# Kernel tuning notes

Hardware: AMD Instinct MI355X
Metric: run time of the kernel (lower is better)

Reference implementation:

```python
import jax, jax.numpy as jnp
import numpy as np

WIN, DIL, PAD, H = 5, 1, 2, 8  # window, dilation, unfold padding, num_heads
C = 256
EPS = 1e-5

def _ln(z, g, b):
    m = jnp.mean(z, axis=-1, keepdims=True)
    v = jnp.mean((z - m) ** 2, axis=-1, keepdims=True)
    return (z - m) * jax.lax.rsqrt(v + EPS) * g + b

def setup_inputs() -> dict:
    key = jax.random.key(0)
    ks = jax.random.split(key, 16)
    s = 0.02
    d = {
        'x': jax.random.normal(ks[0], (32, C, 64, 25), jnp.float32),
        'ln1_g': jnp.ones((C,), jnp.float32), 'ln1_b': jnp.zeros((C,), jnp.float32),
        'q_w': jax.random.normal(ks[1], (C, C)) * s, 'q_b': jnp.zeros((C,)),
        'qa_w': jax.random.normal(ks[2], (C, H)) * s, 'qa_b': jnp.zeros((H,)),
        'k_w': jax.random.normal(ks[3], (C, C)) * s, 'k_b': jnp.zeros((C,)),
        'ka_w': jax.random.normal(ks[4], (C, H)) * s, 'ka_b': jnp.zeros((H,)),
        'v_w': jax.random.normal(ks[5], (C, C)) * s, 'v_b': jnp.zeros((C,)),
        't_w': jax.random.normal(ks[6], (C, C)) * s, 't_b': jnp.zeros((C,)),
        'p_w': jax.random.normal(ks[7], (C, C)) * s, 'p_b': jnp.zeros((C,)),
        'ffn_g': jnp.ones((C,)), 'ffn_b': jnp.zeros((C,)),
        'w1': jax.random.normal(ks[8], (C, C)) * s, 'b1': jnp.zeros((C,)),
        'w2': jax.random.normal(ks[9], (C, C)) * s, 'b2': jnp.zeros((C,)),
    }
    return d

def reference(x, ln1_g, ln1_b, q_w, q_b, qa_w, qa_b, k_w, k_b, ka_w, ka_b,
              v_w, v_b, t_w, t_b, p_w, p_b, ffn_g, ffn_b, w1, b1, w2, b2):
    N, Cc, T, V = x.shape
    hc = Cc // H
    scale = 1.0 / np.sqrt(hc)
    B, L = N * T, WIN * V
    xp = jnp.pad(x, ((0, 0), (0, 0), (PAD, PAD), (0, 0)))
    win = jnp.stack([xp[:, :, k * DIL:k * DIL + T, :] for k in range(WIN)], axis=2)  # (N,C,W,T,V)
    wx = win.transpose(0, 3, 2, 4, 1).reshape(B, L, Cc)
    nx = _ln(wx, ln1_g, ln1_b)
    # attention: softmax-pooled query
    q = nx @ q_w + q_b                                      # (B,L,C)
    qw = jax.nn.softmax(((q @ qa_w + qa_b) * scale).transpose(0, 2, 1), axis=-1)  # (B,H,L)
    qh = q.reshape(B, L, H, hc).transpose(0, 2, 1, 3)       # (B,H,L,hc)
    pq = jnp.einsum('bhl,bhld->bhd', qw, qh)                # (B,H,hc)
    k_ = nx @ k_w + k_b
    kq = k_ * pq.reshape(B, 1, Cc)
    kw = jax.nn.softmax(((kq @ ka_w + ka_b) * scale).transpose(0, 2, 1), axis=-1)
    kh = k_.reshape(B, L, H, hc).transpose(0, 2, 1, 3)
    pk = jnp.einsum('bhl,bhld->bhd', kw, kh)                # (B,H,hc)
    v_ = nx @ v_w + v_b
    vh = v_.reshape(B, L, H, hc).transpose(0, 2, 1, 3)
    kv = (vh * pk[:, :, None, :]).transpose(0, 2, 1, 3).reshape(B, L, Cc)
    kvh = (kv @ t_w + t_b).reshape(B, L, H, hc).transpose(0, 2, 1, 3)
    att = ((kvh + qh).transpose(0, 2, 1, 3).reshape(B, L, Cc)) @ p_w + p_b
    # average over window, residual with flattened x
    att = att.reshape(B, WIN, V, Cc).mean(axis=1)           # (B,V,C)
    att = att + x.transpose(0, 2, 3, 1).reshape(B, V, Cc)
    # FFN residual block
    f = _ln(att, ffn_g, ffn_b)
    f = jax.nn.gelu(f @ w1 + b1, approximate=False) @ w2 + b2
    y = f + att
    return y.reshape(N, T, V, Cc).transpose(0, 3, 1, 2)     # (N,C,T,V)
```

## Files before the change

### kernel.cpp

```cpp
#include <hip/hip_runtime.h>
#include <hip/hip_bf16.h>

typedef unsigned short u16b;
typedef __attribute__((ext_vector_type(8))) short short8;
typedef __attribute__((ext_vector_type(4))) float floatx4;

#define DEV static __device__ __forceinline__

DEV float sh2f(unsigned short s) { union { unsigned u; float f; } c; c.u = ((unsigned)s) << 16; return c.f; }
DEV unsigned short f2b(float f) {
    unsigned u = __float_as_uint(f);
    u += 0x7FFF + ((u >> 16) & 1);
    return (unsigned short)(u >> 16);
}

DEV void gload_lds16(const u16b* g, u16b* l) {
    __builtin_amdgcn_global_load_lds((const __attribute__((address_space(1))) void*)g,
                                     (__attribute__((address_space(3))) void*)l, 16, 0, 0);
}

constexpr int O_LN1G = 0, O_LN1B = 256, O_QB = 512, O_KB = 768, O_VB = 1024,
              O_TB = 1280, O_PB = 1536, O_FFNG = 1792, O_FFNB = 2048,
              O_B1 = 2304, O_B2 = 2560, O_QAB = 2816, O_KAB = 2824,
              O_QAW = 2832, O_KAW = 4880, O_CV = 6928;
constexpr int VALIDC = 51200;

__global__ void detect_k(const unsigned* __restrict__ xw, int* __restrict__ flag) {
    __shared__ int cnt;
    if (threadIdx.x == 0) cnt = 0;
    __syncthreads();
    int my = 0;
    for (int i = threadIdx.x; i < 4096; i += 256) {
        unsigned w = xw[i];
        unsigned e0 = (w >> 7) & 0xFFu;
        if (e0 >= 0xC0u) my++;
    }
    atomicAdd(&cnt, my);
    __syncthreads();
    if (threadIdx.x == 0) flag[0] = (cnt > 64) ? 1 : 0;
}

DEV unsigned short load_cvt(const void* src, size_t idx, int fp32) {
    return fp32 ? f2b(((const float*)src)[idx]) : ((const u16b*)src)[idx];
}

struct VecTab { const void* p[15]; int off[15]; int n[15]; };

__global__ __launch_bounds__(256)
void convert_vecs_k(VecTab tab, const int* __restrict__ flag, u16b* __restrict__ sv) {
    int e = blockIdx.x, fp32 = flag[0];
    const void* s = tab.p[e];
    int n = tab.n[e], off = tab.off[e];
    for (int i = threadIdx.x; i < n; i += 256)
        sv[off + i] = load_cvt(s, i, fp32);
}

struct W8 { const void* p[8]; unsigned dstoff[8]; unsigned rstride[8]; };

__global__ void wtrans_k(W8 tab, u16b* __restrict__ base, const int* __restrict__ flag) {
    __shared__ u16b tile[32][33];
    int fp32 = flag[0];
    const void* src = tab.p[blockIdx.z];
    u16b* dst = base + tab.dstoff[blockIdx.z];
    unsigned rs = tab.rstride[blockIdx.z];
    int c0 = blockIdx.x * 32, r0 = blockIdx.y * 32;
    int tx = threadIdx.x, ty = threadIdx.y;
#pragma unroll
    for (int i = 0; i < 32; i += 8)
        tile[ty + i][tx] = load_cvt(src, (size_t)(r0 + ty + i) * 256 + c0 + tx, fp32);
    __syncthreads();
#pragma unroll
    for (int i = 0; i < 32; i += 8)
        dst[(size_t)(c0 + ty + i) * rs + r0 + tx] = tile[tx][ty + i];
}

__global__ __launch_bounds__(256)
void transpose_in_k(const void* __restrict__ src, u16b* __restrict__ dst,
                    int rows, int cols, const int* __restrict__ flag) {
    __shared__ u16b tile[32][36];
    int fp32 = flag[0];
    int c0 = blockIdx.x * 32, r0 = blockIdx.y * 32;
    size_t zb = (size_t)blockIdx.z * rows * cols;
    int tid = threadIdx.x;
    int r = tid >> 3, c4 = (tid & 7) * 4;
    size_t sidx = zb + (size_t)(r0 + r) * cols + c0 + c4;
    if (fp32) {
        const float4 f4 = *(const float4*)((const float*)src + sidx);
        tile[r][c4]     = f2b(f4.x);
        tile[r][c4 + 1] = f2b(f4.y);
        tile[r][c4 + 2] = f2b(f4.z);
        tile[r][c4 + 3] = f2b(f4.w);
    } else {
        *(ushort4*)&tile[r][c4] = *(const ushort4*)((const u16b*)src + sidx);
    }
    __syncthreads();
    int c = tid >> 3, r4 = (tid & 7) * 4;
    ushort4 o;
    o.x = tile[r4][c]; o.y = tile[r4 + 1][c]; o.z = tile[r4 + 2][c]; o.w = tile[r4 + 3][c];
    *(ushort4*)&dst[zb + (size_t)(c0 + c) * rows + r0 + r4] = o;
}

__global__ __launch_bounds__(256)
void cvec_k(const u16b* __restrict__ pT, u16b* __restrict__ sv) {
    int j = threadIdx.x;
    float acc = sh2f(sv[O_PB + j]);
    const u16b* row = pT + (size_t)j * 256;
    for (int i = 0; i < 256; i += 8) {
        short8 t8 = *(const short8*)&sv[O_TB + i];
        short8 p8 = *(const short8*)&row[i];
#pragma unroll
        for (int u = 0; u < 8; ++u)
            acc += sh2f((unsigned short)t8[u]) * sh2f((unsigned short)p8[u]);
    }
    sv[O_CV + j] = f2b(acc);
}

template <int EPI, int LNA, int XY = 0, int STATS = 0>
__global__ __launch_bounds__(256, 4)
void gemm256(const u16b* __restrict__ A, int aStride, int K,
             const u16b* __restrict__ Wt,
             const u16b* __restrict__ bias, const u16b* __restrict__ addm,
             u16b* __restrict__ out, size_t osParam,
             const float2* __restrict__ stats, const float2* __restrict__ stats2,
             const u16b* __restrict__ gvec, const u16b* __restrict__ bvec,
             float2* __restrict__ statOut, const int* __restrict__ flag) {
    constexpr bool ALDS = (LNA == 0);
    __shared__ u16b As[64 * 72];
    __shared__ u16b Bs[8448];
    __shared__ float sg[256], sb[256];
    const int tid = threadIdx.x;
    const int m0 = (XY ? blockIdx.y : blockIdx.x) * 64;
    const int n0 = (XY ? blockIdx.x : blockIdx.y) * 128;
    const int wv = tid >> 6, lane = tid & 63;
    const int wrow = (wv >> 1) * 32, wcol = (wv & 1) * 64;
    const int fr = lane & 15;
    const int fq = lane >> 4;
    floatx4 acc[2][4];
    const floatx4 zero = {0.f, 0.f, 0.f, 0.f};
#pragma unroll
    for (int i = 0; i < 2; ++i)
#pragma unroll
        for (int j = 0; j < 4; ++j) acc[i][j] = zero;

    float2 strow[2];
    if (LNA) {
        sg[tid] = sh2f(gvec[tid]);
        sb[tid] = sh2f(bvec[tid]);
        if (LNA == 1) {
#pragma unroll
            for (int kk = 0; kk < 2; ++kk) {
                int chunk = tid + kk * 256;
                int row = chunk >> 3, col = (chunk & 7) * 8;
                float s1 = 0.f, s2 = 0.f;
#pragma unroll
                for (int kt2 = 0; kt2 < 256; kt2 += 64) {
                    union { uint4 u; unsigned short h[8]; } rw;
                    rw.u = *(const uint4*)&A[(size_t)(m0 + row) * aStride + kt2 + col];
#pragma unroll
                    for (int j = 0; j < 8; ++j) {
                        float f = sh2f(rw.h[j]);
                        s1 += f; s2 += f * f;
                    }
                }
#pragma unroll
                for (int mm = 1; mm < 8; mm <<= 1) {
                    s1 += __shfl_xor(s1, mm);
                    s2 += __shfl_xor(s2, mm);
                }
                float mean = s1 * (1.f / 256.f);
                float var  = s2 * (1.f / 256.f) - mean * mean;
                strow[kk] = (m0 + row < VALIDC) ? make_float2(mean, rsqrtf(var + 1e-5f))
                                                : make_float2(0.f, 0.f);
            }
        } else {
#pragma unroll
            for (int kk = 0; kk < 2; ++kk) {
                int r = m0 + (tid >> 3) + kk * 32;
                float2 a = stats[r], b = stats2[r];
                float mean = (a.x + b.x) * (1.f / 256.f);
                float var  = (a.y + b.y) * (1.f / 256.f) - mean * mean;
                strow[kk] = make_float2(mean, rsqrtf(var + 1e-5f));
            }
        }
        __syncthreads();
    }

    for (int kt = 0; kt < K; kt += 64) {
        if (ALDS) {
#pragma unroll
            for (int kk = 0; kk < 2; ++kk) {
                int chunk = tid + kk * 256;
                int row = chunk >> 3, col = (chunk & 7) * 8;
                int scol = col ^ ((row & 7) << 3);
                gload_lds16(&A[(size_t)(m0 + row) * aStride + kt + scol], &As[chunk * 8]);
            }
        } else {
#pragma unroll
            for (int kk = 0; kk < 2; ++kk) {
                int chunk = tid + kk * 256;
                int row = chunk >> 3, col = (chunk & 7) * 8;
                union { uint4 u; unsigned short h[8]; } rw;
                rw.u = *(const uint4*)&A[(size_t)(m0 + row) * aStride + kt + col];
#pragma unroll
                for (int j = 0; j < 8; ++j) {
                    float f = sh2f(rw.h[j]);
                    f = (f - strow[kk].x) * strow[kk].y * sg[kt + col + j] + sb[kt + col + j];
                    rw.h[j] = f2b(f);
                }
                *(uint4*)&As[row * 72 + col] = rw.u;
            }
        }
#pragma unroll
        for (int kk = 0; kk < 4; ++kk) {
            int chunk = tid + kk * 256;
            int row = chunk >> 3, col = (chunk & 7) * 8;
            int scol = col ^ ((row & 7) << 3);
            gload_lds16(&Wt[(size_t)(n0 + row) * K + kt + scol], &Bs[chunk * 8]);
        }
        __syncthreads();
#pragma unroll
        for (int s = 0; s < 2; ++s) {
            short8 af[2], bfr[4];
#pragma unroll
            for (int i = 0; i < 2; ++i) {
                int ar = wrow + i * 16 + fr;
                if (ALDS)
                    af[i] = *(const short8*)((const char*)As +
                              ((ar * 128 + s * 64 + fq * 16) ^ ((ar & 7) << 4)));
                else
                    af[i] = *(short8*)&As[ar * 72 + s * 32 + fq * 8];
            }
#pragma unroll
            for (int j = 0; j < 4; ++j) {
                int br = wcol + j * 16 + fr;
                bfr[j] = *(const short8*)((const char*)Bs +
                          ((br * 128 + s * 64 + fq * 16) ^ ((br & 7) << 4)));
            }
#pragma unroll
            for (int i = 0; i < 2; ++i)
#pragma unroll
                for (int j = 0; j < 4; ++j)
                    acc[i][j] = __builtin_amdgcn_mfma_f32_16x16x32_bf16(af[i], bfr[j], acc[i][j], 0, 0, 0);
        }
        __syncthreads();
    }
    float bv[4];
#pragma unroll
    for (int j = 0; j < 4; ++j) bv[j] = bias ? sh2f(bias[n0 + wcol + j * 16 + fr]) : 0.f;

    if (EPI == 5) {
        u16b* CT = Bs;
#pragma unroll
        for (int kk = 0; kk < 4; ++kk) {
            int chunk = tid + kk * 256;
            int row = chunk >> 4, c8 = (chunk & 15) * 8;
            *(uint4*)&CT[row * 132 + c8] = *(const uint4*)&addm[(size_t)(m0 + row) * 256 + n0 + c8];
        }
        __syncthreads();
        int fp32o = flag[0];
#pragma unroll
        for (int i = 0; i < 2; ++i) {
            int lr0 = wrow + i * 16 + fq * 4;
            int row0 = m0 + lr0;
            int n = row0 / 1600;
            int tv = row0 - n * 1600;
#pragma unroll
            for (int j = 0; j < 4; ++j) {
                int lc = wcol + j * 16 + fr;
                int col = n0 + lc;
                float v4[4];
#pragma unroll
                for (int r = 0; r < 4; ++r)
                    v4[r] = acc[i][j][r] + bv[j] + sh2f(CT[(lr0 + r) * 132 + lc]);
                size_t oidx = ((size_t)n * 256 + col) * 1600 + tv;
                if (fp32o) {
                    float4 o = {v4[0], v4[1], v4[2], v4[3]};
                    *(float4*)((float*)out + oidx) = o;
                } else {
                    ushort4 o;
                    o.x = f2b(v4[0]); o.y = f2b(v4[1]); o.z = f2b(v4[2]); o.w = f2b(v4[3]);
                    *(ushort4*)&out[oidx] = o;
                }
            }
        }
    } else if (EPI == 2) {
        float* CTf = (float*)Bs;
#pragma unroll
        for (int half = 0; half < 2; ++half) {
            if ((wrow >> 5) == half) {
#pragma unroll
                for (int i = 0; i < 2; ++i)
#pragma unroll
                    for (int r = 0; r < 4; ++r) {
                        int lrow = i * 16 + fq * 4 + r;
#pragma unroll
                        for (int j = 0; j < 4; ++j)
                            CTf[lrow * 132 + wcol + j * 16 + fr] = acc[i][j][r] + bv[j];
                    }
            }
            __syncthreads();
#pragma unroll
            for (int kk = 0; kk < 2; ++kk) {
                int chunk = tid + kk * 256;
                int row = chunk >> 4, c8 = (chunk & 15) * 8;
                int grow = m0 + half * 32 + row, gcol = n0 + c8;
                union { uint4 u; unsigned short h[8]; } am, ow;
                am.u = *(const uint4*)&addm[(size_t)grow * 256 + gcol];
                float s1 = 0.f, s2 = 0.f;
#pragma unroll
                for (int u8 = 0; u8 < 8; ++u8) {
                    float v = CTf[row * 132 + c8 + u8] + sh2f(am.h[u8]);
                    s1 += v; s2 += v * v;
                    ow.h[u8] = f2b(v);
                }
                if (STATS) {
#pragma unroll
                    for (int mm = 1; mm < 16; mm <<= 1) {
                        s1 += __shfl_xor(s1, mm);
                        s2 += __shfl_xor(s2, mm);
                    }
                    if ((tid & 15) == 0)
                        statOut[(size_t)(n0 >> 7) * 51200 + grow] = make_float2(s1, s2);
                }
                *(uint4*)&out[(size_t)grow * 256 + gcol] = ow.u;
            }
            __syncthreads();
        }
    } else {
        u16b* CT = Bs;
#pragma unroll
        for (int i = 0; i < 2; ++i)
#pragma unroll
            for (int r = 0; r < 4; ++r) {
                int lrow = wrow + i * 16 + fq * 4 + r;
#pragma unroll
                for (int j = 0; j < 4; ++j) {
                    float val = acc[i][j][r] + bv[j];
                    if (EPI == 3) val = 0.5f * val * (1.0f + erff(val * 0.70710678118654752f));
                    CT[lrow * 132 + wcol + j * 16 + fr] = f2b(val);
                }
            }
        __syncthreads();
#pragma unroll
        for (int kk = 0; kk < 4; ++kk) {
            int chunk = tid + kk * 256;
            int row = chunk >> 4, c8 = (chunk & 15) * 8;
            int grow = m0 + row, gcol = n0 + c8;
            uint4 cw = *(const uint4*)&CT[row * 132 + c8];
            if (EPI == 4)      *(uint4*)&out[(size_t)(gcol >> 8) * osParam + (size_t)grow * 256 + (gcol & 255)] = cw;
            else               *(uint4*)&out[(size_t)grow * osParam + gcol] = cw;
        }
    }
}


DEV void logits_union(const u16b* __restrict__ S, const u16b* su, const int* srow,
                      float* slog, const u16b* __restrict__ sv, int aboff, int tid) {
    int wv = tid >> 6, lane = tid & 63;
    int fr = lane & 15, fq = lane >> 4;
    float abv = sh2f(sv[aboff + (fr & 7)]);
    for (int f = wv; f < 10; f += 8) {
        floatx4 acc = {0.f, 0.f, 0.f, 0.f};
        const u16b* Ar = S + (size_t)srow[f * 16 + fr] * 256;
#pragma unroll
        for (int s = 0; s < 8; ++s) {
            short8 a  = *(const short8*)&Ar[s * 32 + fq * 8];
            short8 bb = *(const short8*)&su[fr * 260 + s * 32 + fq * 8];
            acc = __builtin_amdgcn_mfma_f32_16x16x32_bf16(a, bb, acc, 0, 0, 0);
        }
#pragma unroll
        for (int r = 0; r < 4; ++r)
            slog[(f * 16 + fq * 4 + r) * 19 + fr] = (acc[r] + abv) * 0.17677669529663687f;
    }
}

template <int KC>
DEV void softmax16(const float* slog, float* wqA, float* wqB, int tid) {
    int wv = tid >> 6, lane = tid & 63;
#pragma unroll
    for (int c = 0; c < 2; ++c) {
        int combo = wv + c * 8;
        int dt = combo >> 3, h = combo & 7;
        int col = KC ? combo : h;
        const float* src = slog + (size_t)(dt * 25) * 19 + col;
        float v0 = (lane < 125) ? src[lane * 19] : -1e30f;
        float v1 = (lane + 64 < 125) ? src[(lane + 64) * 19] : -1e30f;
        float mx = fmaxf(v0, v1);
#pragma unroll
        for (int o = 32; o; o >>= 1) mx = fmaxf(mx, __shfl_xor(mx, o));
        float e0 = (lane < 125) ? __expf(v0 - mx) : 0.f;
        float e1 = (lane + 64 < 125) ? __expf(v1 - mx) : 0.f;
        float s = e0 + e1;
#pragma unroll
        for (int o = 32; o; o >>= 1) s += __shfl_xor(s, o);
        float inv = 1.f / s;
        float* dst = dt ? wqB : wqA;
        int off = dt ? 25 : 0;
        if (lane < 125) dst[(lane + off) * 9 + h] = e0 * inv;
        if (lane + 64 < 125) dst[(lane + 64 + off) * 9 + h] = e1 * inv;
    }
}

DEV void pool_sweep2(const u16b* __restrict__ S, const int* srow,
                     const float* wqA, const float* wqB,
                     float* scrA, float* scrB, int tid) {
    int c8 = (tid & 31) * 8, h = c8 >> 5, ls = tid >> 5;
    float a0[8] = {0.f,0.f,0.f,0.f,0.f,0.f,0.f,0.f};
    float a1[8] = {0.f,0.f,0.f,0.f,0.f,0.f,0.f,0.f};
    for (int u = ls; u < 150; u += 16) {
        float w0 = wqA[u * 9 + h];
        float w1 = wqB[u * 9 + h];
        short8 d8 = *(const short8*)&S[(size_t)srow[u] * 256 + c8];
#pragma unroll
        for (int j = 0; j < 8; ++j) {
            float f = sh2f((unsigned short)d8[j]);
            a0[j] += w0 * f;
            a1[j] += w1 * f;
        }
    }
#pragma unroll
    for (int j = 0; j < 8; ++j) {
        a0[j] += __shfl_xor(a0[j], 32);
        a1[j] += __shfl_xor(a1[j], 32);
    }
    int wv = tid >> 6, lane = tid & 63;
    if (lane < 32) {
        float4 lo0 = {a0[0], a0[1], a0[2], a0[3]}, hi0 = {a0[4], a0[5], a0[6], a0[7]};
        *(float4*)&scrA[wv * 264 + c8]     = lo0;
        *(float4*)&scrA[wv * 264 + c8 + 4] = hi0;
        float4 lo1 = {a1[0], a1[1], a1[2], a1[3]}, hi1 = {a1[4], a1[5], a1[6], a1[7]};
        *(float4*)&scrB[wv * 260 + c8]     = lo1;
        *(float4*)&scrB[wv * 260 + c8 + 4] = hi1;
    }
}

DEV void pool_reduce2(const float* scrA, const float* scrB,
                      float* out0, float* out1, int tid) {
    if (tid < 256) {
        float s = 0.f;
#pragma unroll
        for (int q = 0; q < 8; ++q) s += scrA[q * 264 + tid];
        out0[tid] = s;
    } else {
        int t2 = tid - 256;
        float s = 0.f;
#pragma unroll
        for (int q = 0; q < 8; ++q) s += scrB[q * 260 + t2];
        out1[t2] = s;
    }
}

DEV void wmean2(const u16b* __restrict__ S, const int* srow,
                const float* scale0, const float* scale1,
                u16b* __restrict__ CB, int base, int nb, int tid) {
    for (int i = tid; i < 800; i += 512) {
        int v = i >> 5, c8 = (i & 31) * 8;
        float s0[8] = {0.f,0.f,0.f,0.f,0.f,0.f,0.f,0.f};
        float s1[8] = {0.f,0.f,0.f,0.f,0.f,0.f,0.f,0.f};
#pragma unroll
        for (int w = 0; w < 6; ++w) {
            short8 d8 = *(const short8*)&S[(size_t)srow[w * 25 + v] * 256 + c8];
#pragma unroll
            for (int j = 0; j < 8; ++j) {
                float f = sh2f((unsigned short)d8[j]);
                if (w < 5)  s0[j] += f;
                if (w >= 1) s1[j] += f;
            }
        }
        unsigned short o0[8], o1[8];
#pragma unroll
        for (int j = 0; j < 8; ++j) {
            float m0 = s0[j] * 0.2f, m1 = s1[j] * 0.2f;
            if (scale0) { m0 *= scale0[c8 + j]; m1 *= scale1[c8 + j]; }
            o0[j] = f2b(m0); o1[j] = f2b(m1);
        }
        *(uint4*)&CB[((size_t)nb * 25 + v) * 512 + base + c8]       = *(uint4*)o0;
        *(uint4*)&CB[((size_t)(nb + 1) * 25 + v) * 512 + base + c8] = *(uint4*)o1;
    }
}

__global__ __launch_bounds__(512)
void pool_fused2(const u16b* __restrict__ qf, const u16b* __restrict__ kf,
                 const u16b* __restrict__ vf, const u16b* __restrict__ sv,
                 u16b* __restrict__ CB) {
    __shared__ int srow[160];
    __shared__ alignas(16) u16b su[16 * 260];
    __shared__ float slog[160 * 19];
    __shared__ float wqA[160 * 9], wqB[160 * 9];
    __shared__ float spq[2][256], spk[2][256];
    int bid = blockIdx.x;
    int b2 = ((bid & 7) << 7) | (bid >> 3);
    int n = b2 >> 5, t0 = (b2 & 31) * 2;
    int nb = n * 64 + t0;
    int tid = threadIdx.x;
    if (tid < 160) {
        int u = tid < 150 ? tid : 149;
        int tl = u / 25, v = u - tl * 25, tt = t0 + tl - 2;
        srow[tid] = ((unsigned)tt < 64u) ? (n * 64 + tt) * 25 + v : 51200;
    }
    for (int i = tid; i < 2048; i += 512) {
        int c = i >> 3, h = i & 7;
        su[h * 260 + c] = sv[O_QAW + i];
    }
    for (int i = tid; i < 1440; i += 512) { wqA[i] = 0.f; wqB[i] = 0.f; }
    __syncthreads();

    logits_union(qf, su, srow, slog, sv, O_QAB, tid);
    __syncthreads();
    softmax16<0>(slog, wqA, wqB, tid);
    __syncthreads();

    pool_sweep2(qf, srow, wqA, wqB, slog, (float*)su, tid);
    wmean2(qf, srow, nullptr, nullptr, CB, 256, nb, tid);
    __syncthreads();
    pool_reduce2(slog, (float*)su, spq[0], spq[1], tid);
    __syncthreads();

    for (int i = tid; i < 4096; i += 512) {
        int c = i >> 4, h16 = i & 15;
        float w = sh2f(sv[O_KAW + c * 8 + (h16 & 7)]) * spq[h16 >> 3][c];
        su[h16 * 260 + c] = f2b(w);
    }
    __syncthreads();

    logits_union(kf, su, srow, slog, sv, O_KAB, tid);
    __syncthreads();
    softmax16<1>(slog, wqA, wqB, tid);
    __syncthreads();

    pool_sweep2(kf, srow, wqA, wqB, slog, (float*)su, tid);
    __syncthreads();
    pool_reduce2(slog, (float*)su, spk[0], spk[1], tid);
    __syncthreads();

    wmean2(vf, srow, spk[0], spk[1], CB, 0, nb, tid);
}

extern "C" void kernel_launch(void* const* d_in, const int* in_sizes, int n_in,
                              void* d_out, int out_size, void* d_ws, size_t ws_size,
                              hipStream_t stream) {
    (void)in_sizes; (void)n_in; (void)out_size; (void)ws_size;
    const void* x    = d_in[0];
    const void* ln1g = d_in[1];  const void* ln1b = d_in[2];
    const void* q_w  = d_in[3];  const void* q_b  = d_in[4];
    const void* qa_w = d_in[5];  const void* qa_b = d_in[6];
    const void* k_w  = d_in[7];  const void* k_b  = d_in[8];
    const void* ka_w = d_in[9];  const void* ka_b = d_in[10];
    const void* v_w  = d_in[11]; const void* v_b  = d_in[12];
    const void* t_w  = d_in[13]; const void* t_b  = d_in[14];
    const void* p_w  = d_in[15]; const void* p_b  = d_in[16];
    const void* ffng = d_in[17]; const void* ffnb = d_in[18];
    const void* w1   = d_in[19]; const void* b1   = d_in[20];
    const void* w2   = d_in[21]; const void* b2   = d_in[22];

    char* ws = (char*)d_ws;
    size_t off = 0;
    auto alloc = [&](size_t bytes) { void* p = ws + off; off += (bytes + 255) & ~(size_t)255; return p; };
    const size_t RPAD = 51328;
    int*    flag = (int*)alloc(256);
    u16b*   sv   = (u16b*)alloc(8192 * 2);
    u16b*   wT   = (u16b*)alloc((size_t)7 * 65536 * 2);
    u16b*   cW   = (u16b*)alloc((size_t)256 * 512 * 2);
    u16b*   xT   = (u16b*)alloc(RPAD * 256 * 2);
    u16b*   Bq   = (u16b*)alloc(RPAD * 256 * 2);
    u16b*   Bk   = (u16b*)alloc(RPAD * 256 * 2);
    u16b*   Bv   = (u16b*)alloc(RPAD * 256 * 2);
    u16b*   CB   = (u16b*)alloc((size_t)51200 * 512 * 2);
    u16b*   att  = (u16b*)alloc((size_t)51200 * 256 * 2);
    float2* st2p = (float2*)alloc((size_t)2 * 51200 * 8);

    u16b* pT  = wT + 3 * 65536;
    u16b* tT  = wT + 4 * 65536;
    u16b* w1T = wT + 5 * 65536;
    u16b* w2T = wT + 6 * 65536;

    detect_k<<<1, 256, 0, stream>>>((const unsigned*)x, flag);
    VecTab tab;
    const void* vp[15] = {ln1g, ln1b, q_b, k_b, v_b, t_b, p_b, ffng, ffnb, b1, b2, qa_b, ka_b, qa_w, ka_w};
    const int vo[15] = {O_LN1G, O_LN1B, O_QB, O_KB, O_VB, O_TB, O_PB, O_FFNG, O_FFNB, O_B1, O_B2, O_QAB, O_KAB, O_QAW, O_KAW};
    const int vn[15] = {256, 256, 256, 256, 256, 256, 256, 256, 256, 256, 256, 8, 8, 2048, 2048};
    for (int i = 0; i < 15; ++i) { tab.p[i] = vp[i]; tab.off[i] = vo[i]; tab.n[i] = vn[i]; }
    convert_vecs_k<<<15, 256, 0, stream>>>(tab, flag, sv);

    dim3 tb(32, 8);
    W8 wt;
    const void* wsrc[8] = {q_w, k_w, v_w, p_w, t_w, w1, w2, p_w};
    for (int i = 0; i < 8; ++i) {
        wt.p[i] = wsrc[i];
        wt.dstoff[i] = (i < 7) ? (unsigned)(i * 65536) : (unsigned)((cW + 256) - wT);
        wt.rstride[i] = (i < 7) ? 256u : 512u;
    }
    wtrans_k<<<dim3(8, 8, 8), tb, 0, stream>>>(wt, wT, flag);
    cvec_k<<<1, 256, 0, stream>>>(pT, sv);
    gemm256<0, 0><<<dim3(4, 2), 256, 0, stream>>>(pT, 256, 256, tT, nullptr, nullptr,
                                                  cW, 512, nullptr, nullptr, nullptr, nullptr,
                                                  nullptr, nullptr);
    transpose_in_k<<<dim3(50, 8, 32), 256, 0, stream>>>(x, xT, 256, 1600, flag);
    gemm256<4, 1, 1><<<dim3(6, 802), 256, 0, stream>>>(xT, 256, 256, wT, sv + O_QB, nullptr,
                                                       Bq, RPAD * 256, nullptr, nullptr,
                                                       sv + O_LN1G, sv + O_LN1B, nullptr, nullptr);
    pool_fused2<<<1024, 512, 0, stream>>>(Bq, Bk, Bv, sv, CB);
    gemm256<2, 0, 1, 1><<<dim3(2, 800), 256, 0, stream>>>(CB, 512, 512, cW, sv + O_CV, xT,
                                                          att, 256, nullptr, nullptr,
                                                          nullptr, nullptr, st2p, nullptr);
    gemm256<3, 2, 1><<<dim3(2, 800), 256, 0, stream>>>(att, 256, 256, w1T, sv + O_B1, nullptr,
                                                       Bq, 256, st2p, st2p + 51200,
                                                       sv + O_FFNG, sv + O_FFNB, nullptr, nullptr);
    gemm256<5, 0, 1><<<dim3(2, 800), 256, 0, stream>>>(Bq, 256, 256, w2T, sv + O_B2, att,
                                                       (u16b*)d_out, 0, nullptr, nullptr,
                                                       nullptr, nullptr, nullptr, flag);
}
```

Measured before the change: 370.8 us.

## Fuse FFN LayerNorm, both GEMMs, GELU and residual into one kernel

Replaces the two separate FFN GEMM launches (LN+W1+GELU, then W2+residual+transposed output) with a single kernel that keeps a 64x256 row tile in LDS. It normalizes att, computes the hidden activations, applies GELU back into LDS, then runs the second GEMM and writes the output. This avoids the round trip of the hidden tensor through global memory and one kernel launch. In exchange each block handles the full 256 output columns, so the grid has fewer, larger blocks with more LDS and registers, which lowers occupancy and re-streams both weight matrices per block.

```diff
diff --git a/kernel.cpp b/kernel.cpp
--- a/kernel.cpp
+++ b/kernel.cpp
@@ -121,9 +121,8 @@
              const u16b* __restrict__ Wt,
              const u16b* __restrict__ bias, const u16b* __restrict__ addm,
              u16b* __restrict__ out, size_t osParam,
-             const float2* __restrict__ stats, const float2* __restrict__ stats2,
              const u16b* __restrict__ gvec, const u16b* __restrict__ bvec,
-             float2* __restrict__ statOut, const int* __restrict__ flag) {
+             float2* __restrict__ statOut) {
     constexpr bool ALDS = (LNA == 0);
     __shared__ u16b As[64 * 72];
     __shared__ u16b Bs[8448];
@@ -146,41 +145,30 @@
     if (LNA) {
         sg[tid] = sh2f(gvec[tid]);
         sb[tid] = sh2f(bvec[tid]);
-        if (LNA == 1) {
-#pragma unroll
-            for (int kk = 0; kk < 2; ++kk) {
-                int chunk = tid + kk * 256;
-                int row = chunk >> 3, col = (chunk & 7) * 8;
-                float s1 = 0.f, s2 = 0.f;
-#pragma unroll
-                for (int kt2 = 0; kt2 < 256; kt2 += 64) {
-                    union { uint4 u; unsigned short h[8]; } rw;
-                    rw.u = *(const uint4*)&A[(size_t)(m0 + row) * aStride + kt2 + col];
-#pragma unroll
-                    for (int j = 0; j < 8; ++j) {
-                        float f = sh2f(rw.h[j]);
-                        s1 += f; s2 += f * f;
-                    }
+#pragma unroll
+        for (int kk = 0; kk < 2; ++kk) {
+            int chunk = tid + kk * 256;
+            int row = chunk >> 3, col = (chunk & 7) * 8;
+            float s1 = 0.f, s2 = 0.f;
+#pragma unroll
+            for (int kt2 = 0; kt2 < 256; kt2 += 64) {
+                union { uint4 u; unsigned short h[8]; } rw;
+                rw.u = *(const uint4*)&A[(size_t)(m0 + row) * aStride + kt2 + col];
+#pragma unroll
+                for (int j = 0; j < 8; ++j) {
+                    float f = sh2f(rw.h[j]);
+                    s1 += f; s2 += f * f;
                 }
-#pragma unroll
-                for (int mm = 1; mm < 8; mm <<= 1) {
-                    s1 += __shfl_xor(s1, mm);
-                    s2 += __shfl_xor(s2, mm);
-                }
-                float mean = s1 * (1.f / 256.f);
-                float var  = s2 * (1.f / 256.f) - mean * mean;
-                strow[kk] = (m0 + row < VALIDC) ? make_float2(mean, rsqrtf(var + 1e-5f))
-                                                : make_float2(0.f, 0.f);
-            }
-        } else {
-#pragma unroll
-            for (int kk = 0; kk < 2; ++kk) {
-                int r = m0 + (tid >> 3) + kk * 32;
-                float2 a = stats[r], b = stats2[r];
-                float mean = (a.x + b.x) * (1.f / 256.f);
-                float var  = (a.y + b.y) * (1.f / 256.f) - mean * mean;
-                strow[kk] = make_float2(mean, rsqrtf(var + 1e-5f));
-            }
+            }
+#pragma unroll
+            for (int mm = 1; mm < 8; mm <<= 1) {
+                s1 += __shfl_xor(s1, mm);
+                s2 += __shfl_xor(s2, mm);
+            }
+            float mean = s1 * (1.f / 256.f);
+            float var  = s2 * (1.f / 256.f) - mean * mean;
+            strow[kk] = (m0 + row < VALIDC) ? make_float2(mean, rsqrtf(var + 1e-5f))
+                                            : make_float2(0.f, 0.f);
         }
         __syncthreads();
     }
@@ -248,16 +236,225 @@
 #pragma unroll
     for (int j = 0; j < 4; ++j) bv[j] = bias ? sh2f(bias[n0 + wcol + j * 16 + fr]) : 0.f;
 
-    if (EPI == 5) {
+    if (EPI == 2) {
+        float* CTf = (float*)Bs;
+#pragma unroll
+        for (int half = 0; half < 2; ++half) {
+            if ((wrow >> 5) == half) {
+#pragma unroll
+                for (int i = 0; i < 2; ++i)
+#pragma unroll
+                    for (int r = 0; r < 4; ++r) {
+                        int lrow = i * 16 + fq * 4 + r;
+#pragma unroll
+                        for (int j = 0; j < 4; ++j)
+                            CTf[lrow * 132 + wcol + j * 16 + fr] = acc[i][j][r] + bv[j];
+                    }
+            }
+            __syncthreads();
+#pragma unroll
+            for (int kk = 0; kk < 2; ++kk) {
+                int chunk = tid + kk * 256;
+                int row = chunk >> 4, c8 = (chunk & 15) * 8;
+                int grow = m0 + half * 32 + row, gcol = n0 + c8;
+                union { uint4 u; unsigned short h[8]; } am, ow;
+                am.u = *(const uint4*)&addm[(size_t)grow * 256 + gcol];
+                float s1 = 0.f, s2 = 0.f;
+#pragma unroll
+                for (int u8 = 0; u8 < 8; ++u8) {
+                    float v = CTf[row * 132 + c8 + u8] + sh2f(am.h[u8]);
+                    s1 += v; s2 += v * v;
+                    ow.h[u8] = f2b(v);
+                }
+                if (STATS) {
+#pragma unroll
+                    for (int mm = 1; mm < 16; mm <<= 1) {
+                        s1 += __shfl_xor(s1, mm);
+                        s2 += __shfl_xor(s2, mm);
+                    }
+                    if ((tid & 15) == 0)
+                        statOut[(size_t)(n0 >> 7) * 51200 + grow] = make_float2(s1, s2);
+                }
+                *(uint4*)&out[(size_t)grow * 256 + gcol] = ow.u;
+            }
+            __syncthreads();
+        }
+    } else {
         u16b* CT = Bs;
+#pragma unroll
+        for (int i = 0; i < 2; ++i)
+#pragma unroll
+            for (int r = 0; r < 4; ++r) {
+                int lrow = wrow + i * 16 + fq * 4 + r;
+#pragma unroll
+                for (int j = 0; j < 4; ++j)
+                    CT[lrow * 132 + wcol + j * 16 + fr] = f2b(acc[i][j][r] + bv[j]);
+            }
+        __syncthreads();
 #pragma unroll
         for (int kk = 0; kk < 4; ++kk) {
             int chunk = tid + kk * 256;
             int row = chunk >> 4, c8 = (chunk & 15) * 8;
-            *(uint4*)&CT[row * 132 + c8] = *(const uint4*)&addm[(size_t)(m0 + row) * 256 + n0 + c8];
-        }
-        __syncthreads();
-        int fp32o = flag[0];
+            int grow = m0 + row, gcol = n0 + c8;
+            uint4 cw = *(const uint4*)&CT[row * 132 + c8];
+            if (EPI == 4)      *(uint4*)&out[(size_t)(gcol >> 8) * osParam + (size_t)grow * 256 + (gcol & 255)] = cw;
+            else               *(uint4*)&out[(size_t)grow * osParam + gcol] = cw;
+        }
+    }
+}
+
+__global__ __launch_bounds__(256, 3)
+void ffn_fused(const u16b* __restrict__ att, const u16b* __restrict__ w1t,
+               const u16b* __restrict__ w2t, const u16b* __restrict__ sv,
+               const float2* __restrict__ stats, const float2* __restrict__ stats2,
+               u16b* __restrict__ out, const int* __restrict__ flag) {
+    __shared__ u16b AT[64 * 264];
+    __shared__ u16b Bs[8448];
+    __shared__ float sg[256], sb[256];
+    const int tid = threadIdx.x;
+    const int m0 = blockIdx.x * 64;
+    const int wv = tid >> 6, lane = tid & 63;
+    const int wrow = (wv >> 1) * 32, wcol = (wv & 1) * 64;
+    const int fr = lane & 15, fq = lane >> 4;
+    const floatx4 zero = {0.f, 0.f, 0.f, 0.f};
+
+    sg[tid] = sh2f(sv[O_FFNG + tid]);
+    sb[tid] = sh2f(sv[O_FFNB + tid]);
+    __syncthreads();
+
+#pragma unroll
+    for (int kk = 0; kk < 8; ++kk) {
+        int chunk = tid + kk * 256;
+        int row = chunk >> 5, col = (chunk & 31) * 8;
+        float2 a = stats[m0 + row], b = stats2[m0 + row];
+        float mean = (a.x + b.x) * (1.f / 256.f);
+        float var  = (a.y + b.y) * (1.f / 256.f) - mean * mean;
+        float rstd = rsqrtf(var + 1e-5f);
+        union { uint4 u; unsigned short h[8]; } rw;
+        rw.u = *(const uint4*)&att[(size_t)(m0 + row) * 256 + col];
+#pragma unroll
+        for (int j = 0; j < 8; ++j) {
+            float f = sh2f(rw.h[j]);
+            f = (f - mean) * rstd * sg[col + j] + sb[col + j];
+            rw.h[j] = f2b(f);
+        }
+        *(uint4*)&AT[row * 264 + col] = rw.u;
+    }
+    __syncthreads();
+
+    floatx4 acc[2][2][4];
+#pragma unroll
+    for (int H = 0; H < 2; ++H)
+#pragma unroll
+        for (int i = 0; i < 2; ++i)
+#pragma unroll
+            for (int j = 0; j < 4; ++j) acc[H][i][j] = zero;
+
+#pragma unroll
+    for (int H = 0; H < 2; ++H) {
+        for (int kt = 0; kt < 256; kt += 64) {
+#pragma unroll
+            for (int kk = 0; kk < 4; ++kk) {
+                int chunk = tid + kk * 256;
+                int row = chunk >> 3, col = (chunk & 7) * 8;
+                int scol = col ^ ((row & 7) << 3);
+                gload_lds16(&w1t[(size_t)(H * 128 + row) * 256 + kt + scol], &Bs[chunk * 8]);
+            }
+            __syncthreads();
+#pragma unroll
+            for (int s = 0; s < 2; ++s) {
+                short8 af[2], bfr[4];
+#pragma unroll
+                for (int i = 0; i < 2; ++i)
+                    af[i] = *(short8*)&AT[(wrow + i * 16 + fr) * 264 + kt + s * 32 + fq * 8];
+#pragma unroll
+                for (int j = 0; j < 4; ++j) {
+                    int br = wcol + j * 16 + fr;
+                    bfr[j] = *(const short8*)((const char*)Bs +
+                              ((br * 128 + s * 64 + fq * 16) ^ ((br & 7) << 4)));
+                }
+#pragma unroll
+                for (int i = 0; i < 2; ++i)
+#pragma unroll
+                    for (int j = 0; j < 4; ++j)
+                        acc[H][i][j] = __builtin_amdgcn_mfma_f32_16x16x32_bf16(af[i], bfr[j], acc[H][i][j], 0, 0, 0);
+            }
+            __syncthreads();
+        }
+    }
+#pragma unroll
+    for (int H = 0; H < 2; ++H) {
+        float bv1[4];
+#pragma unroll
+        for (int j = 0; j < 4; ++j) bv1[j] = sh2f(sv[O_B1 + H * 128 + wcol + j * 16 + fr]);
+#pragma unroll
+        for (int i = 0; i < 2; ++i)
+#pragma unroll
+            for (int r = 0; r < 4; ++r) {
+                int lrow = wrow + i * 16 + fq * 4 + r;
+#pragma unroll
+                for (int j = 0; j < 4; ++j) {
+                    float val = acc[H][i][j][r] + bv1[j];
+                    val = 0.5f * val * (1.0f + erff(val * 0.70710678118654752f));
+                    AT[lrow * 264 + H * 128 + wcol + j * 16 + fr] = f2b(val);
+                }
+            }
+    }
+    __syncthreads();
+
+    floatx4 acc2[2][2][4];
+#pragma unroll
+    for (int H = 0; H < 2; ++H)
+#pragma unroll
+        for (int i = 0; i < 2; ++i)
+#pragma unroll
+            for (int j = 0; j < 4; ++j) acc2[H][i][j] = zero;
+
+#pragma unroll
+    for (int H = 0; H < 2; ++H) {
+        for (int kt = 0; kt < 256; kt += 64) {
+#pragma unroll
+            for (int kk = 0; kk < 4; ++kk) {
+                int chunk = tid + kk * 256;
+                int row = chunk >> 3, col = (chunk & 7) * 8;
+                int scol = col ^ ((row & 7) << 3);
+                gload_lds16(&w2t[(size_t)(H * 128 + row) * 256 + kt + scol], &Bs[chunk * 8]);
+            }
+            __syncthreads();
+#pragma unroll
+            for (int s = 0; s < 2; ++s) {
+                short8 af[2], bfr[4];
+#pragma unroll
+                for (int i = 0; i < 2; ++i)
+                    af[i] = *(short8*)&AT[(wrow + i * 16 + fr) * 264 + kt + s * 32 + fq * 8];
+#pragma unroll
+                for (int j = 0; j < 4; ++j) {
+                    int br = wcol + j * 16 + fr;
+                    bfr[j] = *(const short8*)((const char*)Bs +
+                              ((br * 128 + s * 64 + fq * 16) ^ ((br & 7) << 4)));
+                }
+#pragma unroll
+                for (int i = 0; i < 2; ++i)
+#pragma unroll
+                    for (int j = 0; j < 4; ++j)
+                        acc2[H][i][j] = __builtin_amdgcn_mfma_f32_16x16x32_bf16(af[i], bfr[j], acc2[H][i][j], 0, 0, 0);
+            }
+            __syncthreads();
+        }
+    }
+#pragma unroll
+    for (int kk = 0; kk < 8; ++kk) {
+        int chunk = tid + kk * 256;
+        int row = chunk >> 5, c8 = (chunk & 31) * 8;
+        *(uint4*)&AT[row * 264 + c8] = *(const uint4*)&att[(size_t)(m0 + row) * 256 + c8];
+    }
+    __syncthreads();
+    int fp32o = flag[0];
+#pragma unroll
+    for (int H = 0; H < 2; ++H) {
+        float bv2[4];
+#pragma unroll
+        for (int j = 0; j < 4; ++j) bv2[j] = sh2f(sv[O_B2 + H * 128 + wcol + j * 16 + fr]);
 #pragma unroll
         for (int i = 0; i < 2; ++i) {
             int lr0 = wrow + i * 16 + fq * 4;
@@ -266,13 +463,12 @@
             int tv = row0 - n * 1600;
 #pragma unroll
             for (int j = 0; j < 4; ++j) {
-                int lc = wcol + j * 16 + fr;
-                int col = n0 + lc;
+                int lc = H * 128 + wcol + j * 16 + fr;
                 float v4[4];
 #pragma unroll
                 for (int r = 0; r < 4; ++r)
-                    v4[r] = acc[i][j][r] + bv[j] + sh2f(CT[(lr0 + r) * 132 + lc]);
-                size_t oidx = ((size_t)n * 256 + col) * 1600 + tv;
+                    v4[r] = acc2[H][i][j][r] + bv2[j] + sh2f(AT[(lr0 + r) * 264 + lc]);
+                size_t oidx = ((size_t)n * 256 + lc) * 1600 + tv;
                 if (fp32o) {
                     float4 o = {v4[0], v4[1], v4[2], v4[3]};
                     *(float4*)((float*)out + oidx) = o;
@@ -282,73 +478,6 @@
                     *(ushort4*)&out[oidx] = o;
                 }
             }
-        }
-    } else if (EPI == 2) {
-        float* CTf = (float*)Bs;
-#pragma unroll
-        for (int half = 0; half < 2; ++half) {
-            if ((wrow >> 5) == half) {
-#pragma unroll
-                for (int i = 0; i < 2; ++i)
-#pragma unroll
-                    for (int r = 0; r < 4; ++r) {
-                        int lrow = i * 16 + fq * 4 + r;
-#pragma unroll
-                        for (int j = 0; j < 4; ++j)
-                            CTf[lrow * 132 + wcol + j * 16 + fr] = acc[i][j][r] + bv[j];
-                    }
-            }
-            __syncthreads();
-#pragma unroll
-            for (int kk = 0; kk < 2; ++kk) {
-                int chunk = tid + kk * 256;
-                int row = chunk >> 4, c8 = (chunk & 15) * 8;
-                int grow = m0 + half * 32 + row, gcol = n0 + c8;
-                union { uint4 u; unsigned short h[8]; } am, ow;
-                am.u = *(const uint4*)&addm[(size_t)grow * 256 + gcol];
-                float s1 = 0.f, s2 = 0.f;
-#pragma unroll
-                for (int u8 = 0; u8 < 8; ++u8) {
-                    float v = CTf[row * 132 + c8 + u8] + sh2f(am.h[u8]);
-                    s1 += v; s2 += v * v;
-                    ow.h[u8] = f2b(v);
-                }
-                if (STATS) {
-#pragma unroll
-                    for (int mm = 1; mm < 16; mm <<= 1) {
-                        s1 += __shfl_xor(s1, mm);
-                        s2 += __shfl_xor(s2, mm);
-                    }
-                    if ((tid & 15) == 0)
-                        statOut[(size_t)(n0 >> 7) * 51200 + grow] = make_float2(s1, s2);
-                }
-                *(uint4*)&out[(size_t)grow * 256 + gcol] = ow.u;
-            }
-            __syncthreads();
-        }
-    } else {
-        u16b* CT = Bs;
-#pragma unroll
-        for (int i = 0; i < 2; ++i)
-#pragma unroll
-            for (int r = 0; r < 4; ++r) {
-                int lrow = wrow + i * 16 + fq * 4 + r;
-#pragma unroll
-                for (int j = 0; j < 4; ++j) {
-                    float val = acc[i][j][r] + bv[j];
-                    if (EPI == 3) val = 0.5f * val * (1.0f + erff(val * 0.70710678118654752f));
-                    CT[lrow * 132 + wcol + j * 16 + fr] = f2b(val);
-                }
-            }
-        __syncthreads();
-#pragma unroll
-        for (int kk = 0; kk < 4; ++kk) {
-            int chunk = tid + kk * 256;
-            int row = chunk >> 4, c8 = (chunk & 15) * 8;
-            int grow = m0 + row, gcol = n0 + c8;
-            uint4 cw = *(const uint4*)&CT[row * 132 + c8];
-            if (EPI == 4)      *(uint4*)&out[(size_t)(gcol >> 8) * osParam + (size_t)grow * 256 + (gcol & 255)] = cw;
-            else               *(uint4*)&out[(size_t)grow * osParam + gcol] = cw;
         }
     }
 }
@@ -593,20 +722,14 @@
     wtrans_k<<<dim3(8, 8, 8), tb, 0, stream>>>(wt, wT, flag);
     cvec_k<<<1, 256, 0, stream>>>(pT, sv);
     gemm256<0, 0><<<dim3(4, 2), 256, 0, stream>>>(pT, 256, 256, tT, nullptr, nullptr,
-                                                  cW, 512, nullptr, nullptr, nullptr, nullptr,
-                                                  nullptr, nullptr);
+                                                  cW, 512, nullptr, nullptr, nullptr);
     transpose_in_k<<<dim3(50, 8, 32), 256, 0, stream>>>(x, xT, 256, 1600, flag);
     gemm256<4, 1, 1><<<dim3(6, 802), 256, 0, stream>>>(xT, 256, 256, wT, sv + O_QB, nullptr,
-                                                       Bq, RPAD * 256, nullptr, nullptr,
-                                                       sv + O_LN1G, sv + O_LN1B, nullptr, nullptr);
+                                                       Bq, RPAD * 256,
+                                                       sv + O_LN1G, sv + O_LN1B, nullptr);
     pool_fused2<<<1024, 512, 0, stream>>>(Bq, Bk, Bv, sv, CB);
     gemm256<2, 0, 1, 1><<<dim3(2, 800), 256, 0, stream>>>(CB, 512, 512, cW, sv + O_CV, xT,
-                                                          att, 256, nullptr, nullptr,
-                                                          nullptr, nullptr, st2p, nullptr);
-    gemm256<3, 2, 1><<<dim3(2, 800), 256, 0, stream>>>(att, 256, 256, w1T, sv + O_B1, nullptr,
-                                                       Bq, 256, st2p, st2p + 51200,
-                                                       sv + O_FFNG, sv + O_FFNB, nullptr, nullptr);
-    gemm256<5, 0, 1><<<dim3(2, 800), 256, 0, stream>>>(Bq, 256, 256, w2T, sv + O_B2, att,
-                                                       (u16b*)d_out, 0, nullptr, nullptr,
-                                                       nullptr, nullptr, nullptr, flag);
-}
+                                                          att, 256, nullptr, nullptr, st2p);
+    ffn_fused<<<800, 256, 0, stream>>>(att, w1T, w2T, sv, st2p, st2p + 51200,
+                                       (u16b*)d_out, flag);
+}
```

Measured after the change: 383.7 us. +3.5%, slower.
